# Optimization experiments

Measured on AMD Instinct MI355X. Metric: run time of the kernel, lower is better.

Reference implementation:

```python
import jax, jax.numpy as jnp
import numpy as np

N = 20000      # nodes
E = 320000     # edges (avg degree 16)
IN, HID, OUT, H = 128, 32, 32, 8
NEG_SLOPE = 0.2


def _gat_conv(x, src, dst, W, al, ar, b):
    """One DGL-style GATConv. x: [N, F_in], W: [F_in, H*D], al/ar: [H, D], b: [H*D].
    Returns [N, H, D]."""
    n = x.shape[0]
    Hh, D = al.shape
    feat = (x @ W).reshape(n, Hh, D)                      # [N,H,D]
    el = jnp.sum(feat * al[None], axis=-1)                # [N,H]
    er = jnp.sum(feat * ar[None], axis=-1)                # [N,H]
    e = jax.nn.leaky_relu(el[src] + er[dst], NEG_SLOPE)   # [E,H]
    # edge softmax over incoming edges of each dst node (stable)
    emax = jax.ops.segment_max(e, dst, num_segments=n)    # [N,H]
    ee = jnp.exp(e - emax[dst])                           # [E,H]
    denom = jax.ops.segment_sum(ee, dst, num_segments=n)  # [N,H]
    alpha = ee / denom[dst]                               # [E,H]
    msg = feat[src] * alpha[:, :, None]                   # [E,H,D] gather+weight
    out = jax.ops.segment_sum(msg, dst, num_segments=n)   # [N,H,D] scatter-add
    return out + b.reshape(1, Hh, D)


def setup_inputs() -> dict:
    key = jax.random.key(0)
    ks = jax.random.split(key, 11)
    return {
        "x":   jax.random.normal(ks[0], (N, IN), dtype=jnp.float32),
        "src": jax.random.randint(ks[1], (E,), 0, N, dtype=jnp.int32),
        "dst": jax.random.randint(ks[2], (E,), 0, N, dtype=jnp.int32),
        "W1":  jax.random.normal(ks[3], (IN, H * HID), dtype=jnp.float32) * 0.1,
        "al1": jax.random.normal(ks[4], (H, HID), dtype=jnp.float32) * 0.1,
        "ar1": jax.random.normal(ks[5], (H, HID), dtype=jnp.float32) * 0.1,
        "b1":  jnp.zeros((H * HID,), dtype=jnp.float32),
        "W2":  jax.random.normal(ks[6], (HID, H * OUT), dtype=jnp.float32) * 0.1,
        "al2": jax.random.normal(ks[7], (H, OUT), dtype=jnp.float32) * 0.1,
        "ar2": jax.random.normal(ks[8], (H, OUT), dtype=jnp.float32) * 0.1,
        "b2":  jnp.zeros((H * OUT,), dtype=jnp.float32),
    }


def reference(x, src, dst, W1, al1, ar1, b1, W2, al2, ar2, b2):
    h = _gat_conv(x, src, dst, W1, al1, ar1, b1)          # [N,H,HID]
    h = jnp.mean(jax.nn.relu(h), axis=1)                  # [N,HID]
    h = _gat_conv(h, src, dst, W2, al2, ar2, b2)          # [N,H,OUT]
    return jnp.mean(h, axis=1)                            # [N,OUT]
```

## Files before the change

kernel.cpp:

```cpp
#include <hip/hip_runtime.h>
#include <hip/hip_bf16.h>

#define N_NODES 20000
#define N_EDGES 320000
#define F_IN    128
#define F_HID   32
#define NHEAD   8
#define FDIM    256
#define CAP     96

typedef __hip_bfloat16 bf16;
typedef __attribute__((ext_vector_type(8))) short short8;
typedef __attribute__((ext_vector_type(4))) float f32x4;

__device__ __forceinline__ unsigned short f2bf_rne(float f){
  unsigned u = __float_as_uint(f);
  unsigned r = u + 0x7FFFu + ((u >> 16) & 1u);
  return (unsigned short)(r >> 16);
}
__device__ __forceinline__ float bf2f(unsigned short s){
  return __uint_as_float((unsigned)s << 16);
}

__global__ void fill_bucket_kernel(const int* __restrict__ src, const int* __restrict__ dst,
                                   int* __restrict__ cnt, int* __restrict__ bucket, int e){
  int i = blockIdx.x*256 + threadIdx.x;
  if (i < e){
    int d = dst[i];
    int p = atomicAdd(&cnt[d], 1);
    if (p < CAP) bucket[(size_t)d*CAP + p] = src[i];
  }
}

__global__ void splitT_both_kernel(const float* __restrict__ W1, const float* __restrict__ W2,
                                   unsigned short* __restrict__ h1, unsigned short* __restrict__ l1,
                                   unsigned short* __restrict__ h2, unsigned short* __restrict__ l2){
  int i = blockIdx.x*256 + threadIdx.x;
  const int n1 = FDIM*F_IN;
  if (i < n1){
    int n = i / F_IN, k = i - n*F_IN;
    float v = W1[(size_t)k*FDIM + n];
    unsigned short hs = f2bf_rne(v);
    h1[i] = hs;
    l1[i] = f2bf_rne(v - bf2f(hs));
  } else {
    int j = i - n1;
    int n = j / F_HID, k = j - n*F_HID;
    float v = W2[(size_t)k*FDIM + n];
    unsigned short hs = f2bf_rne(v);
    h2[j] = hs;
    l2[j] = f2bf_rne(v - bf2f(hs));
  }
}

template<int K, int XSPLIT>
__global__ __launch_bounds__(256) void gemm_mfma_kernel(
    const void* __restrict__ Xa, const void* __restrict__ Xb,
    const unsigned short* __restrict__ Wthi, const unsigned short* __restrict__ Wtlo,
    const float* __restrict__ al, const float* __restrict__ ar,
    unsigned short* __restrict__ feat, float* __restrict__ el, float* __restrict__ er)
{
  const int tid  = threadIdx.x;
  const int wv   = tid >> 6;
  const int lane = tid & 63;
  const int quad = lane >> 4;
  const int l16  = lane & 15;
  const int m0   = blockIdx.x * 16;
  constexpr int NC = K / 32;

  short8 Ah[NC], Al_[NC];
  if (XSPLIT){
    const float* xrow = (const float*)Xa + (size_t)(m0 + l16)*K;
    #pragma unroll
    for (int c = 0; c < NC; c++){
      float4 a0 = *(const float4*)(xrow + c*32 + quad*8);
      float4 a1 = *(const float4*)(xrow + c*32 + quad*8 + 4);
      const float vs[8] = {a0.x,a0.y,a0.z,a0.w,a1.x,a1.y,a1.z,a1.w};
      #pragma unroll
      for (int j = 0; j < 8; j++){
        unsigned short hs = f2bf_rne(vs[j]);
        Ah[c][j]  = (short)hs;
        Al_[c][j] = (short)f2bf_rne(vs[j] - bf2f(hs));
      }
    }
  } else {
    const size_t arow = (size_t)(m0 + l16) * K;
    #pragma unroll
    for (int c = 0; c < NC; c++){
      Ah[c]  = *(const short8*)((const unsigned short*)Xa + arow + c*32 + quad*8);
      Al_[c] = *(const short8*)((const unsigned short*)Xb + arow + c*32 + quad*8);
    }
  }

  float elp[8], erp[8];
  #pragma unroll
  for (int j = 0; j < 8; j++){ elp[j] = 0.f; erp[j] = 0.f; }

  #pragma unroll
  for (int t = 0; t < 4; t++){
    const int nc = wv*64 + t*16;
    const size_t brow = (size_t)(nc + l16) * K;
    f32x4 acc = {0.f, 0.f, 0.f, 0.f};
    #pragma unroll
    for (int c = 0; c < NC; c++){
      short8 Bh = *(const short8*)(Wthi + brow + c*32 + quad*8);
      short8 Bl = *(const short8*)(Wtlo + brow + c*32 + quad*8);
      acc = __builtin_amdgcn_mfma_f32_16x16x32_bf16(Ah[c],  Bh, acc, 0, 0, 0);
      acc = __builtin_amdgcn_mfma_f32_16x16x32_bf16(Ah[c],  Bl, acc, 0, 0, 0);
      acc = __builtin_amdgcn_mfma_f32_16x16x32_bf16(Al_[c], Bh, acc, 0, 0, 0);
    }
    const float alv = al[nc + l16];
    const float arv = ar[nc + l16];
    const int hl = t >> 1;
    #pragma unroll
    for (int r = 0; r < 4; r++){
      float v = acc[r];
      feat[(size_t)(m0 + quad*4 + r)*FDIM + nc + l16] = f2bf_rne(v);
      elp[r*2 + hl] = fmaf(v, alv, elp[r*2 + hl]);
      erp[r*2 + hl] = fmaf(v, arv, erp[r*2 + hl]);
    }
  }

  #pragma unroll
  for (int off = 1; off <= 8; off <<= 1){
    #pragma unroll
    for (int j = 0; j < 8; j++){
      elp[j] += __shfl_xor(elp[j], off);
      erp[j] += __shfl_xor(erp[j], off);
    }
  }
  __shared__ float el_lds[16][8], er_lds[16][8];
  if (l16 == 0){
    #pragma unroll
    for (int r = 0; r < 4; r++){
      #pragma unroll
      for (int hl = 0; hl < 2; hl++){
        el_lds[quad*4 + r][wv*2 + hl] = elp[r*2 + hl];
        er_lds[quad*4 + r][wv*2 + hl] = erp[r*2 + hl];
      }
    }
  }
  __syncthreads();
  if (tid < 128){
    int row = tid >> 3, h = tid & 7;
    el[(size_t)(m0 + row)*NHEAD + h] = el_lds[row][h];
    er[(size_t)(m0 + row)*NHEAD + h] = er_lds[row][h];
  }
}

template<int SPLIT_OUT>
__global__ __launch_bounds__(256) void edge_agg_kernel(
    const bf16* __restrict__ feat, const float* __restrict__ el,
    const float* __restrict__ er, const int* __restrict__ cnt,
    const int* __restrict__ bucket, const float* __restrict__ bias,
    float* __restrict__ outp,
    unsigned short* __restrict__ ohi, unsigned short* __restrict__ olo)
{
  const int tid  = threadIdx.x;
  const int wv   = tid >> 6;
  const int lane = tid & 63;
  const int n    = blockIdx.x*4 + wv;

  __shared__ float t_all[4][CAP*9];
  __shared__ int   s_all[4][CAP];
  __shared__ float sum_all[4][NHEAD];
  __shared__ float v_all[4][256];
  float* t_w = t_all[wv];
  int*   s_w = s_all[wv];

  int C = cnt[n];
  if (C > CAP) C = CAP;

  const float4* er4 = (const float4*)(er + (size_t)n*NHEAD);
  float4 era = er4[0], erb = er4[1];
  const float erv[8] = {era.x, era.y, era.z, era.w, erb.x, erb.y, erb.z, erb.w};

  for (int e = lane; e < C; e += 64){
    const int sidx = bucket[(size_t)n*CAP + e];
    s_w[e] = sidx;
    const float4* e4 = (const float4*)(el + (size_t)sidx*NHEAD);
    float4 a = e4[0], bq = e4[1];
    float ev[8] = {a.x, a.y, a.z, a.w, bq.x, bq.y, bq.z, bq.w};
    #pragma unroll
    for (int hh = 0; hh < 8; hh++){
      float v = ev[hh] + erv[hh];
      t_w[e*9 + hh] = (v > 0.f) ? v : 0.2f*v;
    }
  }
  {
    const int h = lane >> 3, d = lane & 7;
    float lm = -INFINITY;
    for (int e = d; e < C; e += 8) lm = fmaxf(lm, t_w[e*9 + h]);
    #pragma unroll
    for (int off = 4; off >= 1; off >>= 1) lm = fmaxf(lm, __shfl_xor(lm, off));
    float ls = 0.f;
    for (int e = d; e < C; e += 8){
      float ex = __expf(t_w[e*9 + h] - lm);
      t_w[e*9 + h] = ex;
      ls += ex;
    }
    #pragma unroll
    for (int off = 4; off >= 1; off >>= 1) ls += __shfl_xor(ls, off);
    if (d == 0) sum_all[wv][h] = ls;
  }

  const int sub = lane >> 5;
  const int l   = lane & 31;
  const int hB  = l >> 2;
  float acc[8] = {0,0,0,0,0,0,0,0};
  for (int e = sub; e < C; e += 2){
    const int sidx = s_w[e];
    const float4 fv = *(const float4*)(feat + (size_t)sidx*FDIM + (l << 3));
    const float w = t_w[e*9 + hB];
    const unsigned* u = (const unsigned*)&fv;
    #pragma unroll
    for (int j = 0; j < 4; j++){
      float flo = __uint_as_float(u[j] << 16);
      float fhi = __uint_as_float(u[j] & 0xFFFF0000u);
      acc[2*j]   = fmaf(w, flo, acc[2*j]);
      acc[2*j+1] = fmaf(w, fhi, acc[2*j+1]);
    }
  }
  #pragma unroll
  for (int j = 0; j < 8; j++) acc[j] += __shfl_xor(acc[j], 32);

  if (lane < 32){
    const float s = sum_all[wv][l >> 2];
    const float4* b4 = (const float4*)(bias + (l << 3));
    float4 ba = b4[0], bb = b4[1];
    float bv[8] = {ba.x, ba.y, ba.z, ba.w, bb.x, bb.y, bb.z, bb.w};
    float v[8];
    #pragma unroll
    for (int j = 0; j < 8; j++){
      float val = (C > 0) ? (acc[j] / s) : 0.f;
      val += bv[j];
      if (SPLIT_OUT) val = fmaxf(val, 0.f);
      v[j] = val;
    }
    float4* v4 = (float4*)&v_all[wv][l << 3];
    v4[0] = make_float4(v[0], v[1], v[2], v[3]);
    v4[1] = make_float4(v[4], v[5], v[6], v[7]);
  }
  if (lane < 32){
    float sum = 0.f;
    #pragma unroll
    for (int hh = 0; hh < 8; hh++) sum += v_all[wv][hh*32 + lane];
    sum *= 0.125f;
    if (SPLIT_OUT){
      unsigned short hs = f2bf_rne(sum);
      ohi[(size_t)n*32 + lane] = hs;
      olo[(size_t)n*32 + lane] = f2bf_rne(sum - bf2f(hs));
    } else {
      outp[(size_t)n*32 + lane] = sum;
    }
  }
}

extern "C" void kernel_launch(void* const* d_in, const int* in_sizes, int n_in,
                              void* d_out, int out_size, void* d_ws, size_t ws_size,
                              hipStream_t stream)
{
  const float* x   = (const float*)d_in[0];
  const int*   src = (const int*)  d_in[1];
  const int*   dst = (const int*)  d_in[2];
  const float* W1  = (const float*)d_in[3];
  const float* al1 = (const float*)d_in[4];
  const float* ar1 = (const float*)d_in[5];
  const float* b1  = (const float*)d_in[6];
  const float* W2  = (const float*)d_in[7];
  const float* al2 = (const float*)d_in[8];
  const float* ar2 = (const float*)d_in[9];
  const float* b2  = (const float*)d_in[10];
  (void)in_sizes; (void)n_in; (void)out_size; (void)ws_size;

  size_t o = 0;
  char* base = (char*)d_ws;
  auto take = [&](size_t bytes) -> char* {
    char* p = base + o;
    o += (bytes + 255) & ~(size_t)255;
    return p;
  };
  unsigned short* feat  = (unsigned short*)take((size_t)N_NODES*FDIM*2);
  float* el     = (float*)take((size_t)N_NODES*NHEAD*4);
  float* er     = (float*)take((size_t)N_NODES*NHEAD*4);
  int*   cnt    = (int*)  take((size_t)N_NODES*4);
  int*   bucket = (int*)  take((size_t)N_NODES*CAP*4);
  unsigned short* Hhi  = (unsigned short*)take((size_t)N_NODES*F_HID*2);
  unsigned short* Hlo  = (unsigned short*)take((size_t)N_NODES*F_HID*2);
  unsigned short* W1th = (unsigned short*)take((size_t)FDIM*F_IN*2);
  unsigned short* W1tl = (unsigned short*)take((size_t)FDIM*F_IN*2);
  unsigned short* W2th = (unsigned short*)take((size_t)FDIM*F_HID*2);
  unsigned short* W2tl = (unsigned short*)take((size_t)FDIM*F_HID*2);

  hipMemsetAsync(cnt, 0, (size_t)N_NODES*4, stream);
  fill_bucket_kernel<<<(N_EDGES+255)/256, 256, 0, stream>>>(src, dst, cnt, bucket, N_EDGES);
  splitT_both_kernel<<<(FDIM*(F_IN+F_HID))/256, 256, 0, stream>>>(
      W1, W2, W1th, W1tl, W2th, W2tl);

  gemm_mfma_kernel<F_IN, 1><<<N_NODES/16, 256, 0, stream>>>(
      x, nullptr, W1th, W1tl, al1, ar1, feat, el, er);
  edge_agg_kernel<1><<<N_NODES/4, 256, 0, stream>>>(
      (const bf16*)feat, el, er, cnt, bucket, b1, nullptr, Hhi, Hlo);

  gemm_mfma_kernel<F_HID, 0><<<N_NODES/16, 256, 0, stream>>>(
      Hhi, Hlo, W2th, W2tl, al2, ar2, feat, el, er);
  edge_agg_kernel<0><<<N_NODES/4, 256, 0, stream>>>(
      (const bf16*)feat, el, er, cnt, bucket, b2, (float*)d_out, nullptr, nullptr);
}
```

Before: 197.8 us.

## Merge prep kernels, split el gather across lanes, prefetch feature rows

Merges the bucket-fill and weight-split kernels into one launch by partitioning block indices, removing one kernel launch. In the edge aggregation kernel, the el gather now uses two lanes per edge, each loading one float4, so more lanes take part when degree is small. The feature gather loop is software-pipelined so the next edge's row load is issued before the current FMAs, hiding memory latency at the cost of extra registers.

```diff
diff --git a/kernel.cpp b/kernel.cpp
--- a/kernel.cpp
+++ b/kernel.cpp
@@ -22,34 +22,38 @@
   return __uint_as_float((unsigned)s << 16);
 }
 
-__global__ void fill_bucket_kernel(const int* __restrict__ src, const int* __restrict__ dst,
-                                   int* __restrict__ cnt, int* __restrict__ bucket, int e){
-  int i = blockIdx.x*256 + threadIdx.x;
-  if (i < e){
-    int d = dst[i];
-    int p = atomicAdd(&cnt[d], 1);
-    if (p < CAP) bucket[(size_t)d*CAP + p] = src[i];
-  }
-}
-
-__global__ void splitT_both_kernel(const float* __restrict__ W1, const float* __restrict__ W2,
-                                   unsigned short* __restrict__ h1, unsigned short* __restrict__ l1,
-                                   unsigned short* __restrict__ h2, unsigned short* __restrict__ l2){
-  int i = blockIdx.x*256 + threadIdx.x;
-  const int n1 = FDIM*F_IN;
-  if (i < n1){
-    int n = i / F_IN, k = i - n*F_IN;
-    float v = W1[(size_t)k*FDIM + n];
-    unsigned short hs = f2bf_rne(v);
-    h1[i] = hs;
-    l1[i] = f2bf_rne(v - bf2f(hs));
+#define FILLB  ((N_EDGES + 255) / 256)
+#define SPLITB ((FDIM * (F_IN + F_HID)) / 256)
+__global__ void prep_kernel(const int* __restrict__ src, const int* __restrict__ dst,
+                            int* __restrict__ cnt, int* __restrict__ bucket,
+                            const float* __restrict__ W1, const float* __restrict__ W2,
+                            unsigned short* __restrict__ h1, unsigned short* __restrict__ l1,
+                            unsigned short* __restrict__ h2, unsigned short* __restrict__ l2){
+  const int b = blockIdx.x;
+  if (b < FILLB){
+    int i = b*256 + threadIdx.x;
+    if (i < N_EDGES){
+      int d = dst[i];
+      int p = atomicAdd(&cnt[d], 1);
+      if (p < CAP) bucket[(size_t)d*CAP + p] = src[i];
+    }
   } else {
-    int j = i - n1;
-    int n = j / F_HID, k = j - n*F_HID;
-    float v = W2[(size_t)k*FDIM + n];
-    unsigned short hs = f2bf_rne(v);
-    h2[j] = hs;
-    l2[j] = f2bf_rne(v - bf2f(hs));
+    int i = (b - FILLB)*256 + threadIdx.x;
+    const int n1 = FDIM*F_IN;
+    if (i < n1){
+      int n = i / F_IN, k = i - n*F_IN;
+      float v = W1[(size_t)k*FDIM + n];
+      unsigned short hs = f2bf_rne(v);
+      h1[i] = hs;
+      l1[i] = f2bf_rne(v - bf2f(hs));
+    } else {
+      int j = i - n1;
+      int n = j / F_HID, k = j - n*F_HID;
+      float v = W2[(size_t)k*FDIM + n];
+      unsigned short hs = f2bf_rne(v);
+      h2[j] = hs;
+      l2[j] = f2bf_rne(v - bf2f(hs));
+    }
   }
 }
 
@@ -175,16 +179,16 @@
   float4 era = er4[0], erb = er4[1];
   const float erv[8] = {era.x, era.y, era.z, era.w, erb.x, erb.y, erb.z, erb.w};
 
-  for (int e = lane; e < C; e += 64){
+  for (int idx = lane; idx < C*2; idx += 64){
+    const int e = idx >> 1, j = idx & 1;
     const int sidx = bucket[(size_t)n*CAP + e];
-    s_w[e] = sidx;
-    const float4* e4 = (const float4*)(el + (size_t)sidx*NHEAD);
-    float4 a = e4[0], bq = e4[1];
-    float ev[8] = {a.x, a.y, a.z, a.w, bq.x, bq.y, bq.z, bq.w};
-    #pragma unroll
-    for (int hh = 0; hh < 8; hh++){
-      float v = ev[hh] + erv[hh];
-      t_w[e*9 + hh] = (v > 0.f) ? v : 0.2f*v;
+    if (j == 0) s_w[e] = sidx;
+    float4 a = ((const float4*)(el + (size_t)sidx*NHEAD))[j];
+    const float ev[4] = {a.x, a.y, a.z, a.w};
+    #pragma unroll
+    for (int hh = 0; hh < 4; hh++){
+      float v = ev[hh] + erv[j*4 + hh];
+      t_w[e*9 + j*4 + hh] = (v > 0.f) ? v : 0.2f*v;
     }
   }
   {
@@ -207,10 +211,15 @@
   const int sub = lane >> 5;
   const int l   = lane & 31;
   const int hB  = l >> 2;
+  const int coff = l << 3;
   float acc[8] = {0,0,0,0,0,0,0,0};
-  for (int e = sub; e < C; e += 2){
-    const int sidx = s_w[e];
-    const float4 fv = *(const float4*)(feat + (size_t)sidx*FDIM + (l << 3));
+  int e = sub;
+  float4 fv;
+  if (e < C) fv = *(const float4*)(feat + (size_t)s_w[e]*FDIM + coff);
+  while (e < C){
+    const int en = e + 2;
+    float4 fnext;
+    if (en < C) fnext = *(const float4*)(feat + (size_t)s_w[en]*FDIM + coff);
     const float w = t_w[e*9 + hB];
     const unsigned* u = (const unsigned*)&fv;
     #pragma unroll
@@ -220,13 +229,15 @@
       acc[2*j]   = fmaf(w, flo, acc[2*j]);
       acc[2*j+1] = fmaf(w, fhi, acc[2*j+1]);
     }
+    fv = fnext;
+    e = en;
   }
   #pragma unroll
   for (int j = 0; j < 8; j++) acc[j] += __shfl_xor(acc[j], 32);
 
   if (lane < 32){
     const float s = sum_all[wv][l >> 2];
-    const float4* b4 = (const float4*)(bias + (l << 3));
+    const float4* b4 = (const float4*)(bias + coff);
     float4 ba = b4[0], bb = b4[1];
     float bv[8] = {ba.x, ba.y, ba.z, ba.w, bb.x, bb.y, bb.z, bb.w};
     float v[8];
@@ -237,7 +248,7 @@
       if (SPLIT_OUT) val = fmaxf(val, 0.f);
       v[j] = val;
     }
-    float4* v4 = (float4*)&v_all[wv][l << 3];
+    float4* v4 = (float4*)&v_all[wv][coff];
     v4[0] = make_float4(v[0], v[1], v[2], v[3]);
     v4[1] = make_float4(v[4], v[5], v[6], v[7]);
   }
@@ -293,9 +304,8 @@
   unsigned short* W2tl = (unsigned short*)take((size_t)FDIM*F_HID*2);
 
   hipMemsetAsync(cnt, 0, (size_t)N_NODES*4, stream);
-  fill_bucket_kernel<<<(N_EDGES+255)/256, 256, 0, stream>>>(src, dst, cnt, bucket, N_EDGES);
-  splitT_both_kernel<<<(FDIM*(F_IN+F_HID))/256, 256, 0, stream>>>(
-      W1, W2, W1th, W1tl, W2th, W2tl);
+  prep_kernel<<<FILLB + SPLITB, 256, 0, stream>>>(
+      src, dst, cnt, bucket, W1, W2, W1th, W1tl, W2th, W2tl);
 
   gemm_mfma_kernel<F_IN, 1><<<N_NODES/16, 256, 0, stream>>>(
       x, nullptr, W1th, W1tl, al1, ar1, feat, el, er);
```

Result: no change. 197.5 us (-0.2%).
